# Optimization experiments

Hardware: AMD Instinct MI355X
Metric: run time of the kernel (lower is better)

## Reference

```python
import jax, jax.numpy as jnp
import numpy as np

B, N, FEAT, HID, CTX = 16384, 7, 512, 256, 256
COMB = N * HID + CTX  # 2048


def setup_inputs() -> dict:
    key = jax.random.key(0)
    ks = jax.random.split(key, 20)
    s = lambda k, shape, sc=0.05: jax.random.normal(k, shape, dtype=jnp.float32) * sc
    adj = jax.random.randint(ks[1], (N, N), 0, 2).astype(jnp.float32)
    # guarantee self-loops so no row is fully masked (still exercise nan_to_num path robustly)
    adj = jnp.maximum(adj, jnp.eye(N, dtype=jnp.float32))
    return {
        "node_feats": jax.random.normal(ks[0], (B, N, FEAT), dtype=jnp.float32),
        "adj": adj,
        "context": jax.random.normal(ks[2], (B, CTX), dtype=jnp.float32),
        "base_preds": jax.random.normal(ks[3], (B, 5), dtype=jnp.float32),
        "W1": s(ks[4], (HID, FEAT)),
        "a1": s(ks[5], (1, 2 * HID)),
        "W2": s(ks[6], (HID, HID)),
        "a2": s(ks[7], (1, 2 * HID)),
        "wh1_w": s(ks[8], (32, COMB)), "wh1_b": s(ks[9], (32,)),
        "wh2_w": s(ks[10], (16, 32)), "wh2_b": s(ks[11], (16,)),
        "wh3_w": s(ks[12], (5, 16)), "wh3_b": s(ks[13], (5,)),
        "rh1_w": s(ks[14], (16, COMB)), "rh1_b": s(ks[15], (16,)),
        "rh2_w": s(ks[16], (1, 16)), "rh2_b": s(ks[17], (1,)),
    }


def _gat_layer(x, adj, W, a):
    # x: (B, N, in_dim); W: (D, in_dim); a: (1, 2D)
    h = jnp.einsum('bni,di->bnd', x, W)  # (B, N, D)
    D = W.shape[0]
    # a([h_i, h_j]) == h_i @ a[:, :D] + h_j @ a[:, D:]
    s_i = h @ a[0, :D]   # (B, N)
    s_j = h @ a[0, D:]   # (B, N)
    e = s_i[:, :, None] + s_j[:, None, :]          # (B, N, N)
    e = jax.nn.leaky_relu(e, negative_slope=0.2)
    e = jnp.where(adj[None] == 0, -jnp.inf, e)
    alpha = jax.nn.softmax(e, axis=-1)
    alpha = jnp.nan_to_num(alpha, nan=0.0)
    out = jnp.einsum('bij,bjd->bid', alpha, h)     # (B, N, D)
    return out, alpha


def reference(node_feats, adj, context, base_preds, W1, a1, W2, a2,
              wh1_w, wh1_b, wh2_w, wh2_b, wh3_w, wh3_b,
              rh1_w, rh1_b, rh2_w, rh2_b):
    h, _attn1 = _gat_layer(node_feats, adj, W1, a1)
    h = jax.nn.relu(h)
    h, attn2 = _gat_layer(h, adj, W2, a2)
    h = jax.nn.relu(h)
    graph_embed = h.reshape(h.shape[0], -1)                 # (B, N*D)
    combined = jnp.concatenate([graph_embed, context], -1)  # (B, COMB)
    # weight head (dropout is inference-mode identity)
    t = jax.nn.relu(combined @ wh1_w.T + wh1_b)
    t = jax.nn.relu(t @ wh2_w.T + wh2_b)
    raw_weights = t @ wh3_w.T + wh3_b                       # (B, 5)
    weights = jax.nn.softmax(raw_weights, axis=-1)
    weighted_pred = jnp.sum(weights * base_preds, axis=-1)  # (B,)
    r = jnp.tanh(combined @ rh1_w.T + rh1_b)
    residual = (r @ rh2_w.T + rh2_b)[:, 0] * 0.05
    pred = jnp.maximum(weighted_pred + residual, 0.05)
    return pred, weights, attn2
```

## Files before the change

### kernel.cpp

```cpp
#include <hip/hip_runtime.h>

#define B_SZ 16384
#define NN 7
#define HID 256
#define COMB 2048

typedef __attribute__((ext_vector_type(8))) short short8;
typedef __attribute__((ext_vector_type(4))) float floatx4;
typedef __attribute__((ext_vector_type(4))) unsigned short ushortx4;
typedef unsigned short us;

__device__ __forceinline__ float bf2f(us u) {
    union { unsigned int i; float f; } v; v.i = ((unsigned int)u) << 16; return v.f;
}
__device__ __forceinline__ us f2bf(float f) {
    union { unsigned int i; float f; } v; v.f = f;
    return (us)((v.i + 0x7FFFu + ((v.i >> 16) & 1u)) >> 16);
}
__device__ __forceinline__ us f2bf_fast(float f) {
    union { unsigned int i; float f; } v; v.f = f;
    return (us)((v.i + 0x8000u) >> 16);
}

__device__ __forceinline__ void bar_lds() {
    asm volatile("s_waitcnt lgkmcnt(0)" ::: "memory");
    __builtin_amdgcn_s_barrier();
}

__device__ __forceinline__ int hoff(int r, int k8) {
    return ((r >> 3) << 8) | ((r & 7) << 5) | (k8 & 24) | ((k8 ^ r) & 7);
}
__device__ __forceinline__ int aoff(int r, int k8) {
    return ((r >> 3) << 6) | ((r & 7) << 3) | ((k8 ^ r) & 7);
}

__global__ __launch_bounds__(256) void pack_weights(const float* __restrict__ W1,
                                                    const float* __restrict__ W2,
                                                    const float* __restrict__ wh1,
                                                    const float* __restrict__ rh1,
                                                    us* __restrict__ dst) {
    int i = (blockIdx.x * 256 + threadIdx.x) * 4;
    if (i >= 294912) return;
    const float* src; int off;
    if (i < 131072)      { src = W1;  off = i; }
    else if (i < 196608) { src = W2;  off = i - 131072; }
    else if (i < 262144) { src = wh1; off = i - 196608; }
    else                 { src = rh1; off = i - 262144; }
    floatx4 v = *(const floatx4*)(src + off);
    ushortx4 o = {f2bf(v[0]), f2bf(v[1]), f2bf(v[2]), f2bf(v[3])};
    *(ushortx4*)(dst + i) = o;
}

template <bool WRITE_ALPHA>
__device__ __forceinline__ void attn_graph(us* hs, int r0, const float* adjs, const float* avec,
                                           float* alpha_dst, int lane) {
    const int k8 = lane >> 1, sub = (lane & 1) * 4;
    float hv[NN][4];
#pragma unroll
    for (int n = 0; n < NN; ++n) {
        ushortx4 rr = *(const ushortx4*)(hs + hoff(r0 + n, k8) * 8 + sub);
        hv[n][0] = bf2f(rr[0]); hv[n][1] = bf2f(rr[1]);
        hv[n][2] = bf2f(rr[2]); hv[n][3] = bf2f(rr[3]);
    }
    floatx4 ai = *(const floatx4*)(avec + lane * 4);
    floatx4 aj = *(const floatx4*)(avec + HID + lane * 4);
    float si[NN], sj[NN];
#pragma unroll
    for (int n = 0; n < NN; ++n) {
        float pi = hv[n][0] * ai[0] + hv[n][1] * ai[1] + hv[n][2] * ai[2] + hv[n][3] * ai[3];
        float pj = hv[n][0] * aj[0] + hv[n][1] * aj[1] + hv[n][2] * aj[2] + hv[n][3] * aj[3];
#pragma unroll
        for (int off = 32; off; off >>= 1) {
            pi += __shfl_xor(pi, off);
            pj += __shfl_xor(pj, off);
        }
        si[n] = pi; sj[n] = pj;
    }
    const int j = lane & 7;
    float sjm = sj[0];
    if (j == 1) sjm = sj[1];
    if (j == 2) sjm = sj[2];
    if (j == 3) sjm = sj[3];
    if (j == 4) sjm = sj[4];
    if (j == 5) sjm = sj[5];
    if (j == 6) sjm = sj[6];
    const int jc = (j < 7) ? j : 0;
    float alpha[NN];
#pragma unroll
    for (int i = 0; i < NN; ++i) {
        float x = si[i] + sjm;
        x = (x >= 0.f) ? x : 0.2f * x;
        bool ok = (j < 7) && (adjs[i * 7 + jc] != 0.f);
        float e = ok ? x : -1e30f;
        float m = e;
        m = fmaxf(m, __shfl_xor(m, 1, 8));
        m = fmaxf(m, __shfl_xor(m, 2, 8));
        m = fmaxf(m, __shfl_xor(m, 4, 8));
        float ex = ok ? __expf(e - m) : 0.f;
        float s = ex;
        s += __shfl_xor(s, 1, 8);
        s += __shfl_xor(s, 2, 8);
        s += __shfl_xor(s, 4, 8);
        alpha[i] = (s > 0.f) ? ex * __frcp_rn(s) : 0.f;
    }
    if (WRITE_ALPHA && lane < 7) {
#pragma unroll
        for (int i = 0; i < NN; ++i) alpha_dst[i * NN + lane] = alpha[i];
    }
#pragma unroll
    for (int i = 0; i < NN; ++i) {
        floatx4 o = (floatx4){0.f, 0.f, 0.f, 0.f};
#pragma unroll
        for (int jj = 0; jj < NN; ++jj) {
            float a = __shfl(alpha[i], jj, 8);
            o[0] += a * hv[jj][0]; o[1] += a * hv[jj][1];
            o[2] += a * hv[jj][2]; o[3] += a * hv[jj][3];
        }
        ushortx4 st = {f2bf(fmaxf(o[0], 0.f)), f2bf(fmaxf(o[1], 0.f)),
                       f2bf(fmaxf(o[2], 0.f)), f2bf(fmaxf(o[3], 0.f))};
        *(ushortx4*)(hs + hoff(r0 + i, k8) * 8 + sub) = st;
    }
}

__device__ __forceinline__ void cwrite(us* hs, floatx4 (&acc)[4][2], int wave, int quad, int m16) {
#pragma unroll
    for (int rt = 0; rt < 4; ++rt)
#pragma unroll
        for (int ct = 0; ct < 2; ++ct)
#pragma unroll
            for (int i = 0; i < 4; ++i) {
                int row = rt * 16 + quad * 4 + i;
                if (row < 56)
                    hs[hoff(row, wave * 4 + ct * 2 + (m16 >> 3)) * 8 + (m16 & 7)] =
                        f2bf(acc[rt][ct][i]);
            }
}

__global__ __launch_bounds__(512, 4) void fused_all(
    const float* __restrict__ Af, const us* __restrict__ W1b, const us* __restrict__ W2b,
    const us* __restrict__ Whb, const float* __restrict__ adj, const float* __restrict__ a1v,
    const float* __restrict__ a2v, const float* __restrict__ context,
    const float* __restrict__ wh1_b, const float* __restrict__ wh2_w,
    const float* __restrict__ wh2_b, const float* __restrict__ wh3_w,
    const float* __restrict__ wh3_b, const float* __restrict__ rh1_b,
    const float* __restrict__ rh2_w, const float* __restrict__ rh2_b,
    const float* __restrict__ base_preds, float* __restrict__ out) {
    __shared__ __attribute__((aligned(16))) us hs[16384];
    __shared__ __attribute__((aligned(16))) char ubuf[16384];
    __shared__ float adjs[52];
    us* As = (us*)ubuf;
    float* red = (float*)ubuf;
    float* fin = red + 3072;
    const int tid = threadIdx.x;
    const int wave = tid >> 6, lane = tid & 63;
    const int quad = lane >> 4, m16 = lane & 15;
    const long gbase = (long)blockIdx.x * 8;
    if (tid < 49) adjs[tid] = adj[tid];
    *(ushortx4*)(hs + 14336 + tid * 4) = (ushortx4){0, 0, 0, 0};

    floatx4 acc[4][2];
#pragma unroll
    for (int rt = 0; rt < 4; ++rt)
#pragma unroll
        for (int ct = 0; ct < 2; ++ct) acc[rt][ct] = (floatx4){0.f, 0.f, 0.f, 0.f};

    const int r = tid >> 3, kq8 = tid & 7;
    long rowA = gbase * 7 + r; if (rowA > 114687) rowA = 114687;
    const float* aptr = Af + rowA * 512 + kq8 * 8;
    us* wdst = As + aoff(r, kq8) * 8;
    const int colb = wave * 32;

    floatx4 v0 = *(const floatx4*)aptr;
    floatx4 v1 = *(const floatx4*)(aptr + 4);
#pragma unroll
    for (int s = 0; s < 8; ++s) {
        short8 sv;
        sv[0] = f2bf_fast(v0[0]); sv[1] = f2bf_fast(v0[1]);
        sv[2] = f2bf_fast(v0[2]); sv[3] = f2bf_fast(v0[3]);
        sv[4] = f2bf_fast(v1[0]); sv[5] = f2bf_fast(v1[1]);
        sv[6] = f2bf_fast(v1[2]); sv[7] = f2bf_fast(v1[3]);
        if (s < 7) {
            v0 = *(const floatx4*)(aptr + (s + 1) * 64);
            v1 = *(const floatx4*)(aptr + (s + 1) * 64 + 4);
        }
        *(short8*)(wdst + (s & 1) * 4096) = sv;
        bar_lds();
        const us* Ab = As + (s & 1) * 4096;
        const int k0 = s * 64;
#pragma unroll
        for (int t = 0; t < 2; ++t) {
            short8 b0 = *(const short8*)(W1b + (long)(colb + m16) * 512 + k0 + t * 32 + quad * 8);
            short8 b1 = *(const short8*)(W1b + (long)(colb + 16 + m16) * 512 + k0 + t * 32 + quad * 8);
            short8 a[4];
#pragma unroll
            for (int rt = 0; rt < 4; ++rt)
                a[rt] = *(const short8*)(Ab + aoff(rt * 16 + m16, t * 4 + quad) * 8);
#pragma unroll
            for (int rt = 0; rt < 4; ++rt) {
                acc[rt][0] = __builtin_amdgcn_mfma_f32_16x16x32_bf16(a[rt], b0, acc[rt][0], 0, 0, 0);
                acc[rt][1] = __builtin_amdgcn_mfma_f32_16x16x32_bf16(a[rt], b1, acc[rt][1], 0, 0, 0);
            }
        }
    }
    cwrite(hs, acc, wave, quad, m16);
    bar_lds();
    attn_graph<false>(hs, wave * NN, adjs, a1v, nullptr, lane);
    bar_lds();

#pragma unroll
    for (int rt = 0; rt < 4; ++rt)
#pragma unroll
        for (int ct = 0; ct < 2; ++ct) acc[rt][ct] = (floatx4){0.f, 0.f, 0.f, 0.f};
#pragma unroll
    for (int s = 0; s < 4; ++s) {
        const int k0 = s * 64;
#pragma unroll
        for (int t = 0; t < 2; ++t) {
            short8 b0 = *(const short8*)(W2b + (long)(colb + m16) * 256 + k0 + t * 32 + quad * 8);
            short8 b1 = *(const short8*)(W2b + (long)(colb + 16 + m16) * 256 + k0 + t * 32 + quad * 8);
            short8 a[4];
#pragma unroll
            for (int rt = 0; rt < 4; ++rt)
                a[rt] = *(const short8*)(hs + hoff(rt * 16 + m16, s * 8 + t * 4 + quad) * 8);
#pragma unroll
            for (int rt = 0; rt < 4; ++rt) {
                acc[rt][0] = __builtin_amdgcn_mfma_f32_16x16x32_bf16(a[rt], b0, acc[rt][0], 0, 0, 0);
                acc[rt][1] = __builtin_amdgcn_mfma_f32_16x16x32_bf16(a[rt], b1, acc[rt][1], 0, 0, 0);
            }
        }
    }
    bar_lds();
    cwrite(hs, acc, wave, quad, m16);
    bar_lds();
    attn_graph<true>(hs, wave * NN, adjs, a2v, out + 6 * B_SZ + (gbase + wave) * 49, lane);
    bar_lds();

    floatx4 acc3[3];
#pragma unroll
    for (int ct = 0; ct < 3; ++ct) acc3[ct] = (floatx4){0.f, 0.f, 0.f, 0.f};
    const int g = m16 & 7;
#pragma unroll
    for (int s2 = 0; s2 < 8; ++s2) {
        const int kk = s2 * 32;
        short8 a;
        if (wave < 7) {
            a = *(const short8*)(hs + hoff(g * NN + wave, s2 * 4 + quad) * 8);
        } else {
            const float* cp = context + (gbase + g) * 256 + kk + quad * 8;
            floatx4 c0 = *(const floatx4*)cp;
            floatx4 c1 = *(const floatx4*)(cp + 4);
            a[0] = (short)f2bf(c0[0]); a[1] = (short)f2bf(c0[1]);
            a[2] = (short)f2bf(c0[2]); a[3] = (short)f2bf(c0[3]);
            a[4] = (short)f2bf(c1[0]); a[5] = (short)f2bf(c1[1]);
            a[6] = (short)f2bf(c1[2]); a[7] = (short)f2bf(c1[3]);
        }
#pragma unroll
        for (int ct = 0; ct < 3; ++ct) {
            short8 bh = *(const short8*)(Whb + (long)(ct * 16 + m16) * COMB + wave * 256 + kk + quad * 8);
            acc3[ct] = __builtin_amdgcn_mfma_f32_16x16x32_bf16(a, bh, acc3[ct], 0, 0, 0);
        }
    }
#pragma unroll
    for (int ct = 0; ct < 3; ++ct)
#pragma unroll
        for (int i = 0; i < 4; ++i) {
            int g2 = quad * 4 + i;
            if (g2 < 8) red[wave * 384 + g2 * 48 + ct * 16 + m16] = acc3[ct][i];
        }
    bar_lds();
    if (tid < 384) {
        float ssum = 0.f;
#pragma unroll
        for (int w = 0; w < 8; ++w) ssum += red[w * 384 + tid];
        fin[tid] = ssum;
    }
    bar_lds();

    const int fj = lane & 7, fg = lane >> 3;
    const long fb = gbase + fg;
    float rp = 0.f;
    float* t1s = red;
    float* t2s = red + 256;
    if (tid < 64) {
        const float* g48 = fin + fg * 48;
#pragma unroll
        for (int x = 0; x < 4; ++x) {
            int k = fj * 4 + x;
            t1s[fg * 32 + k] = fmaxf(g48[k] + wh1_b[k], 0.f);
        }
#pragma unroll
        for (int x = 0; x < 2; ++x) {
            int k = fj * 2 + x;
            float rv = tanhf(g48[32 + k] + rh1_b[k]);
            rp += rh2_w[k] * rv;
        }
    }
    bar_lds();
    if (tid < 64) {
        float s0 = wh2_b[fj * 2], s1 = wh2_b[fj * 2 + 1];
#pragma unroll
        for (int k = 0; k < 32; ++k) {
            float tv = t1s[fg * 32 + k];
            s0 += wh2_w[(fj * 2) * 32 + k] * tv;
            s1 += wh2_w[(fj * 2 + 1) * 32 + k] * tv;
        }
        t2s[fg * 16 + fj * 2] = fmaxf(s0, 0.f);
        t2s[fg * 16 + fj * 2 + 1] = fmaxf(s1, 0.f);
    }
    bar_lds();
    if (tid < 64) {
        float rw = -1e30f;
        if (fj < 5) {
            float s = wh3_b[fj];
#pragma unroll
            for (int k = 0; k < 16; ++k) s += wh3_w[fj * 16 + k] * t2s[fg * 16 + k];
            rw = s;
        }
        float m = rw;
        m = fmaxf(m, __shfl_xor(m, 1, 8));
        m = fmaxf(m, __shfl_xor(m, 2, 8));
        m = fmaxf(m, __shfl_xor(m, 4, 8));
        float e = (fj < 5) ? __expf(rw - m) : 0.f;
        float se = e;
        se += __shfl_xor(se, 1, 8);
        se += __shfl_xor(se, 2, 8);
        se += __shfl_xor(se, 4, 8);
        float inv = 1.f / se;
        float wp = 0.f;
        if (fj < 5) {
            float w = e * inv;
            out[B_SZ + fb * 5 + fj] = w;
            wp = w * base_preds[fb * 5 + fj];
        }
        wp += __shfl_xor(wp, 1, 8);
        wp += __shfl_xor(wp, 2, 8);
        wp += __shfl_xor(wp, 4, 8);
        float rs = rp;
        rs += __shfl_xor(rs, 1, 8);
        rs += __shfl_xor(rs, 2, 8);
        rs += __shfl_xor(rs, 4, 8);
        if (fj == 0) out[fb] = fmaxf(wp + (rs + rh2_b[0]) * 0.05f, 0.05f);
    }
}

extern "C" void kernel_launch(void* const* d_in, const int* in_sizes, int n_in,
                              void* d_out, int out_size, void* d_ws, size_t ws_size,
                              hipStream_t stream) {
    const float* node_feats = (const float*)d_in[0];
    const float* adj        = (const float*)d_in[1];
    const float* context    = (const float*)d_in[2];
    const float* base_preds = (const float*)d_in[3];
    const float* W1         = (const float*)d_in[4];
    const float* a1         = (const float*)d_in[5];
    const float* W2         = (const float*)d_in[6];
    const float* a2         = (const float*)d_in[7];
    const float* wh1_w = (const float*)d_in[8];
    const float* wh1_b = (const float*)d_in[9];
    const float* wh2_w = (const float*)d_in[10];
    const float* wh2_b = (const float*)d_in[11];
    const float* wh3_w = (const float*)d_in[12];
    const float* wh3_b = (const float*)d_in[13];
    const float* rh1_w = (const float*)d_in[14];
    const float* rh1_b = (const float*)d_in[15];
    const float* rh2_w = (const float*)d_in[16];
    const float* rh2_b = (const float*)d_in[17];
    float* out = (float*)d_out;

    char* ws = (char*)d_ws;
    us* W1b = (us*)ws;
    us* W2b = W1b + 131072;
    us* Whb = W2b + 65536;

    pack_weights<<<288, 256, 0, stream>>>(W1, W2, wh1_w, rh1_w, W1b);

    fused_all<<<2048, 512, 0, stream>>>(node_feats, W1b, W2b, Whb, adj, a1, a2, context,
                                        wh1_b, wh2_w, wh2_b, wh3_w, wh3_b,
                                        rh1_b, rh2_w, rh2_b, base_preds, out);
}
```

Baseline: 523.0 us.

## Halve block to 4 graphs with 256 threads and retile MFMA per wave

Each block now handles 4 graphs (28 rows) with 4 waves instead of 8 graphs with 8 waves, doubling the grid. Each wave computes 64 output columns over 2 row tiles instead of 32 columns over 4 row tiles, which cuts padded MFMA rows (32 vs 64 for 28/56 real rows). The head GEMM loops over two slices per wave, with zero rows padding the 16-row tile. Shared memory per block is halved, which should allow more resident blocks. The cost is that weight B-fragments are reloaded by twice as many blocks and more of the head MFMA lanes are idle.

```diff
diff --git a/kernel.cpp b/kernel.cpp
--- a/kernel.cpp
+++ b/kernel.cpp
@@ -122,21 +122,21 @@
     }
 }
 
-__device__ __forceinline__ void cwrite(us* hs, floatx4 (&acc)[4][2], int wave, int quad, int m16) {
-#pragma unroll
-    for (int rt = 0; rt < 4; ++rt)
-#pragma unroll
-        for (int ct = 0; ct < 2; ++ct)
+__device__ __forceinline__ void cwrite(us* hs, floatx4 (&acc)[2][4], int wave, int quad, int m16) {
+#pragma unroll
+    for (int rt = 0; rt < 2; ++rt)
+#pragma unroll
+        for (int ct = 0; ct < 4; ++ct)
 #pragma unroll
             for (int i = 0; i < 4; ++i) {
                 int row = rt * 16 + quad * 4 + i;
-                if (row < 56)
-                    hs[hoff(row, wave * 4 + ct * 2 + (m16 >> 3)) * 8 + (m16 & 7)] =
+                if (row < 28)
+                    hs[hoff(row, wave * 8 + ct * 2 + (m16 >> 3)) * 8 + (m16 & 7)] =
                         f2bf(acc[rt][ct][i]);
             }
 }
 
-__global__ __launch_bounds__(512, 4) void fused_all(
+__global__ __launch_bounds__(256, 4) void fused_all(
     const float* __restrict__ Af, const us* __restrict__ W1b, const us* __restrict__ W2b,
     const us* __restrict__ Whb, const float* __restrict__ adj, const float* __restrict__ a1v,
     const float* __restrict__ a2v, const float* __restrict__ context,
@@ -145,30 +145,29 @@
     const float* __restrict__ wh3_b, const float* __restrict__ rh1_b,
     const float* __restrict__ rh2_w, const float* __restrict__ rh2_b,
     const float* __restrict__ base_preds, float* __restrict__ out) {
-    __shared__ __attribute__((aligned(16))) us hs[16384];
-    __shared__ __attribute__((aligned(16))) char ubuf[16384];
+    __shared__ __attribute__((aligned(16))) us hs[8192];
+    __shared__ __attribute__((aligned(16))) char ubuf[8192];
     __shared__ float adjs[52];
     us* As = (us*)ubuf;
     float* red = (float*)ubuf;
-    float* fin = red + 3072;
+    float* fin = red + 768;
     const int tid = threadIdx.x;
     const int wave = tid >> 6, lane = tid & 63;
     const int quad = lane >> 4, m16 = lane & 15;
-    const long gbase = (long)blockIdx.x * 8;
+    const long gbase = (long)blockIdx.x * 4;
     if (tid < 49) adjs[tid] = adj[tid];
-    *(ushortx4*)(hs + 14336 + tid * 4) = (ushortx4){0, 0, 0, 0};
-
-    floatx4 acc[4][2];
-#pragma unroll
-    for (int rt = 0; rt < 4; ++rt)
-#pragma unroll
-        for (int ct = 0; ct < 2; ++ct) acc[rt][ct] = (floatx4){0.f, 0.f, 0.f, 0.f};
+    *(ushortx4*)(hs + 7168 + tid * 4) = (ushortx4){0, 0, 0, 0};
+
+    floatx4 acc[2][4];
+#pragma unroll
+    for (int rt = 0; rt < 2; ++rt)
+#pragma unroll
+        for (int ct = 0; ct < 4; ++ct) acc[rt][ct] = (floatx4){0.f, 0.f, 0.f, 0.f};
 
     const int r = tid >> 3, kq8 = tid & 7;
     long rowA = gbase * 7 + r; if (rowA > 114687) rowA = 114687;
     const float* aptr = Af + rowA * 512 + kq8 * 8;
     us* wdst = As + aoff(r, kq8) * 8;
-    const int colb = wave * 32;
 
     floatx4 v0 = *(const floatx4*)aptr;
     floatx4 v1 = *(const floatx4*)(aptr + 4);
@@ -183,22 +182,22 @@
             v0 = *(const floatx4*)(aptr + (s + 1) * 64);
             v1 = *(const floatx4*)(aptr + (s + 1) * 64 + 4);
         }
-        *(short8*)(wdst + (s & 1) * 4096) = sv;
+        *(short8*)(wdst + (s & 1) * 2048) = sv;
         bar_lds();
-        const us* Ab = As + (s & 1) * 4096;
+        const us* Ab = As + (s & 1) * 2048;
         const int k0 = s * 64;
 #pragma unroll
         for (int t = 0; t < 2; ++t) {
-            short8 b0 = *(const short8*)(W1b + (long)(colb + m16) * 512 + k0 + t * 32 + quad * 8);
-            short8 b1 = *(const short8*)(W1b + (long)(colb + 16 + m16) * 512 + k0 + t * 32 + quad * 8);
-            short8 a[4];
-#pragma unroll
-            for (int rt = 0; rt < 4; ++rt)
-                a[rt] = *(const short8*)(Ab + aoff(rt * 16 + m16, t * 4 + quad) * 8);
-#pragma unroll
-            for (int rt = 0; rt < 4; ++rt) {
-                acc[rt][0] = __builtin_amdgcn_mfma_f32_16x16x32_bf16(a[rt], b0, acc[rt][0], 0, 0, 0);
-                acc[rt][1] = __builtin_amdgcn_mfma_f32_16x16x32_bf16(a[rt], b1, acc[rt][1], 0, 0, 0);
+            short8 b[4];
+#pragma unroll
+            for (int ct = 0; ct < 4; ++ct)
+                b[ct] = *(const short8*)(W1b + (long)(wave * 64 + ct * 16 + m16) * 512 + k0 + t * 32 + quad * 8);
+            short8 a0 = *(const short8*)(Ab + aoff(m16, t * 4 + quad) * 8);
+            short8 a1 = *(const short8*)(Ab + aoff(16 + m16, t * 4 + quad) * 8);
+#pragma unroll
+            for (int ct = 0; ct < 4; ++ct) {
+                acc[0][ct] = __builtin_amdgcn_mfma_f32_16x16x32_bf16(a0, b[ct], acc[0][ct], 0, 0, 0);
+                acc[1][ct] = __builtin_amdgcn_mfma_f32_16x16x32_bf16(a1, b[ct], acc[1][ct], 0, 0, 0);
             }
         }
     }
@@ -208,24 +207,24 @@
     bar_lds();
 
 #pragma unroll
-    for (int rt = 0; rt < 4; ++rt)
-#pragma unroll
-        for (int ct = 0; ct < 2; ++ct) acc[rt][ct] = (floatx4){0.f, 0.f, 0.f, 0.f};
+    for (int rt = 0; rt < 2; ++rt)
+#pragma unroll
+        for (int ct = 0; ct < 4; ++ct) acc[rt][ct] = (floatx4){0.f, 0.f, 0.f, 0.f};
 #pragma unroll
     for (int s = 0; s < 4; ++s) {
         const int k0 = s * 64;
 #pragma unroll
         for (int t = 0; t < 2; ++t) {
-            short8 b0 = *(const short8*)(W2b + (long)(colb + m16) * 256 + k0 + t * 32 + quad * 8);
-            short8 b1 = *(const short8*)(W2b + (long)(colb + 16 + m16) * 256 + k0 + t * 32 + quad * 8);
-            short8 a[4];
-#pragma unroll
-            for (int rt = 0; rt < 4; ++rt)
-                a[rt] = *(const short8*)(hs + hoff(rt * 16 + m16, s * 8 + t * 4 + quad) * 8);
-#pragma unroll
-            for (int rt = 0; rt < 4; ++rt) {
-                acc[rt][0] = __builtin_amdgcn_mfma_f32_16x16x32_bf16(a[rt], b0, acc[rt][0], 0, 0, 0);
-                acc[rt][1] = __builtin_amdgcn_mfma_f32_16x16x32_bf16(a[rt], b1, acc[rt][1], 0, 0, 0);
+            short8 b[4];
+#pragma unroll
+            for (int ct = 0; ct < 4; ++ct)
+                b[ct] = *(const short8*)(W2b + (long)(wave * 64 + ct * 16 + m16) * 256 + k0 + t * 32 + quad * 8);
+            short8 a0 = *(const short8*)(hs + hoff(m16, s * 8 + t * 4 + quad) * 8);
+            short8 a1 = *(const short8*)(hs + hoff(16 + m16, s * 8 + t * 4 + quad) * 8);
+#pragma unroll
+            for (int ct = 0; ct < 4; ++ct) {
+                acc[0][ct] = __builtin_amdgcn_mfma_f32_16x16x32_bf16(a0, b[ct], acc[0][ct], 0, 0, 0);
+                acc[1][ct] = __builtin_amdgcn_mfma_f32_16x16x32_bf16(a1, b[ct], acc[1][ct], 0, 0, 0);
             }
         }
     }
@@ -238,26 +237,33 @@
     floatx4 acc3[3];
 #pragma unroll
     for (int ct = 0; ct < 3; ++ct) acc3[ct] = (floatx4){0.f, 0.f, 0.f, 0.f};
-    const int g = m16 & 7;
-#pragma unroll
-    for (int s2 = 0; s2 < 8; ++s2) {
-        const int kk = s2 * 32;
-        short8 a;
-        if (wave < 7) {
-            a = *(const short8*)(hs + hoff(g * NN + wave, s2 * 4 + quad) * 8);
-        } else {
-            const float* cp = context + (gbase + g) * 256 + kk + quad * 8;
-            floatx4 c0 = *(const floatx4*)cp;
-            floatx4 c1 = *(const floatx4*)(cp + 4);
-            a[0] = (short)f2bf(c0[0]); a[1] = (short)f2bf(c0[1]);
-            a[2] = (short)f2bf(c0[2]); a[3] = (short)f2bf(c0[3]);
-            a[4] = (short)f2bf(c1[0]); a[5] = (short)f2bf(c1[1]);
-            a[6] = (short)f2bf(c1[2]); a[7] = (short)f2bf(c1[3]);
-        }
-#pragma unroll
-        for (int ct = 0; ct < 3; ++ct) {
-            short8 bh = *(const short8*)(Whb + (long)(ct * 16 + m16) * COMB + wave * 256 + kk + quad * 8);
-            acc3[ct] = __builtin_amdgcn_mfma_f32_16x16x32_bf16(a, bh, acc3[ct], 0, 0, 0);
+    const int g = m16 & 3;
+#pragma unroll
+    for (int sl2 = 0; sl2 < 2; ++sl2) {
+        const int sl = wave * 2 + sl2;
+#pragma unroll
+        for (int s2 = 0; s2 < 8; ++s2) {
+            const int kk = s2 * 32;
+            short8 a;
+            if (sl < 7) {
+                int row = (m16 < 4) ? (g * NN + sl) : 28;
+                a = *(const short8*)(hs + hoff(row, s2 * 4 + quad) * 8);
+            } else if (m16 < 4) {
+                const float* cp = context + (gbase + g) * 256 + kk + quad * 8;
+                floatx4 c0 = *(const floatx4*)cp;
+                floatx4 c1 = *(const floatx4*)(cp + 4);
+                a[0] = (short)f2bf(c0[0]); a[1] = (short)f2bf(c0[1]);
+                a[2] = (short)f2bf(c0[2]); a[3] = (short)f2bf(c0[3]);
+                a[4] = (short)f2bf(c1[0]); a[5] = (short)f2bf(c1[1]);
+                a[6] = (short)f2bf(c1[2]); a[7] = (short)f2bf(c1[3]);
+            } else {
+                a = (short8){0, 0, 0, 0, 0, 0, 0, 0};
+            }
+#pragma unroll
+            for (int ct = 0; ct < 3; ++ct) {
+                short8 bh = *(const short8*)(Whb + (long)(ct * 16 + m16) * COMB + sl * 256 + kk + quad * 8);
+                acc3[ct] = __builtin_amdgcn_mfma_f32_16x16x32_bf16(a, bh, acc3[ct], 0, 0, 0);
+            }
         }
     }
 #pragma unroll
@@ -265,23 +271,23 @@
 #pragma unroll
         for (int i = 0; i < 4; ++i) {
             int g2 = quad * 4 + i;
-            if (g2 < 8) red[wave * 384 + g2 * 48 + ct * 16 + m16] = acc3[ct][i];
-        }
-    bar_lds();
-    if (tid < 384) {
+            if (g2 < 4) red[wave * 192 + g2 * 48 + ct * 16 + m16] = acc3[ct][i];
+        }
+    bar_lds();
+    if (tid < 192) {
         float ssum = 0.f;
 #pragma unroll
-        for (int w = 0; w < 8; ++w) ssum += red[w * 384 + tid];
+        for (int w = 0; w < 4; ++w) ssum += red[w * 192 + tid];
         fin[tid] = ssum;
     }
     bar_lds();
 
-    const int fj = lane & 7, fg = lane >> 3;
+    const int fj = tid & 7, fg = (tid >> 3) & 3;
     const long fb = gbase + fg;
     float rp = 0.f;
     float* t1s = red;
-    float* t2s = red + 256;
-    if (tid < 64) {
+    float* t2s = red + 128;
+    if (tid < 32) {
         const float* g48 = fin + fg * 48;
 #pragma unroll
         for (int x = 0; x < 4; ++x) {
@@ -296,7 +302,7 @@
         }
     }
     bar_lds();
-    if (tid < 64) {
+    if (tid < 32) {
         float s0 = wh2_b[fj * 2], s1 = wh2_b[fj * 2 + 1];
 #pragma unroll
         for (int k = 0; k < 32; ++k) {
@@ -308,7 +314,7 @@
         t2s[fg * 16 + fj * 2 + 1] = fmaxf(s1, 0.f);
     }
     bar_lds();
-    if (tid < 64) {
+    if (tid < 32) {
         float rw = -1e30f;
         if (fj < 5) {
             float s = wh3_b[fj];
@@ -373,7 +379,7 @@
 
     pack_weights<<<288, 256, 0, stream>>>(W1, W2, wh1_w, rh1_w, W1b);
 
-    fused_all<<<2048, 512, 0, stream>>>(node_feats, W1b, W2b, Whb, adj, a1, a2, context,
+    fused_all<<<4096, 256, 0, stream>>>(node_feats, W1b, W2b, Whb, adj, a1, a2, context,
                                         wh1_b, wh2_w, wh2_b, wh3_w, wh3_b,
                                         rh1_b, rh2_w, rh2_b, base_preds, out);
 }
```

Result: slower. 621.0 us (+18.7%).
